# Kernel optimization log

Measured on AMD Instinct MI355X. Metric: run time of the kernel, lower is better.

## Reference

```python
import jax, jax.numpy as jnp
import numpy as np

M, N1, N2, DX, H = 4, 1024, 1024, 3, 64


def setup_inputs() -> dict:
    key = jax.random.key(0)
    ks = jax.random.split(key, 8)
    diff = jax.random.normal(ks[0], (M, N1, N2, DX), dtype=jnp.float32)
    mask = jax.random.randint(ks[1], (M, N1, N2), 0, 2) == 1  # True -> masked out
    W1 = jax.random.normal(ks[2], (DX, H), dtype=jnp.float32) / np.float32(np.sqrt(DX))
    b1 = jnp.zeros((H,), jnp.float32)
    W2 = jax.random.normal(ks[3], (H, H), dtype=jnp.float32) / np.float32(np.sqrt(H))
    b2 = jnp.zeros((H,), jnp.float32)
    W3 = jax.random.normal(ks[4], (H, 1), dtype=jnp.float32) / np.float32(np.sqrt(H))
    b3 = jnp.zeros((1,), jnp.float32)
    return {"diff": diff, "mask": mask, "W1": W1, "b1": b1,
            "W2": W2, "b2": b2, "W3": W3, "b3": b3}


def reference(diff, mask, W1, b1, W2, b2, W3, b3):
    # MLP applied pointwise over [m, n1, n2, dx] -> scalar score per (m, n1, n2)
    h = jax.nn.relu(jnp.einsum("mijd,dh->mijh", diff, W1) + b1)
    h = jax.nn.relu(jnp.einsum("mijh,hk->mijk", h, W2) + b2)
    dots = (jnp.einsum("mijh,ho->mijo", h, W3) + b3)[..., 0]  # [m, n1, n2]
    # masked_fill(mask, -inf) then softmax over n2
    dots = jnp.where(mask, -jnp.inf, dots)
    return jax.nn.softmax(dots, axis=-1)
```

## Files before the change

### kernel.cpp

```cpp
#include <hip/hip_runtime.h>
#include <hip/hip_fp16.h>
#include <math.h>

typedef __attribute__((ext_vector_type(8))) _Float16 half8;
typedef __attribute__((ext_vector_type(2))) __fp16 fp16x2;
typedef __attribute__((ext_vector_type(4))) float float4v;

#define MFMA_F16 __builtin_amdgcn_mfma_f32_16x16x32_f16

__global__ __launch_bounds__(256, 2) void mlp_softmax_kernel(
    const float* __restrict__ diff, const int* __restrict__ mask,
    const float* __restrict__ W1, const float* __restrict__ b1,
    const float* __restrict__ W2, const float* __restrict__ b2,
    const float* __restrict__ W3, float* __restrict__ out)
{
    __shared__ float s_diff[3072];
    __shared__ float s_w2[4096];
    __shared__ float s_w1[192];
    __shared__ float s_b1[64];
    __shared__ float s_b2[64];
    __shared__ float s_w3[64];
    __shared__ float s_dots[1024];
    __shared__ float s_red[8];

    const int tid = threadIdx.x;
    const int bid = blockIdx.x;
    const long row_off = (long)bid * 3072;

    {
        const float4v* gd = (const float4v*)(diff + row_off);
        float4v* sd = (float4v*)s_diff;
        #pragma unroll
        for (int it = 0; it < 3; ++it) sd[tid + 256 * it] = gd[tid + 256 * it];
        const float4v* gw2 = (const float4v*)W2;
        float4v* sw2 = (float4v*)s_w2;
        #pragma unroll
        for (int it = 0; it < 4; ++it) sw2[tid + 256 * it] = gw2[tid + 256 * it];
        if (tid < 48)                    ((float4v*)s_w1)[tid]      = ((const float4v*)W1)[tid];
        else if (tid >= 64 && tid < 80)  ((float4v*)s_b1)[tid - 64] = ((const float4v*)b1)[tid - 64];
        else if (tid >= 80 && tid < 96)  ((float4v*)s_b2)[tid - 80] = ((const float4v*)b2)[tid - 80];
        else if (tid >= 96 && tid < 112) ((float4v*)s_w3)[tid - 96] = ((const float4v*)W3)[tid - 96];
    }
    __syncthreads();

    const int lane = tid & 63;
    const int wv   = tid >> 6;
    const int lg   = lane >> 4;
    const int lr   = lane & 15;

    float w1r[2][3][8], b1r[2][8];
    #pragma unroll
    for (int kh = 0; kh < 2; ++kh) {
        const int hb = kh * 32 + lg * 8;
        #pragma unroll
        for (int e = 0; e < 8; ++e) {
            b1r[kh][e] = s_b1[hb + e];
            #pragma unroll
            for (int d = 0; d < 3; ++d) w1r[kh][d][e] = s_w1[d * 64 + hb + e];
        }
    }
    half8 bfr[4][2];
    #pragma unroll
    for (int nt = 0; nt < 4; ++nt) {
        #pragma unroll
        for (int kh = 0; kh < 2; ++kh) {
            union { fp16x2 h2[4]; half8 h8; } u;
            #pragma unroll
            for (int ep = 0; ep < 4; ++ep) {
                const int k0 = kh * 32 + lg * 8 + ep * 2;
                const float f0 = s_w2[(k0    ) * 64 + nt * 16 + lr];
                const float f1 = s_w2[(k0 + 1) * 64 + nt * 16 + lr];
                u.h2[ep] = __builtin_amdgcn_cvt_pkrtz(f0, f1);
            }
            bfr[nt][kh] = u.h8;
        }
    }
    float b2r[4], w3r[4];
    #pragma unroll
    for (int nt = 0; nt < 4; ++nt) {
        b2r[nt] = s_b2[nt * 16 + lr];
        w3r[nt] = s_w3[nt * 16 + lr];
    }

    const int jw0 = wv * 256;
    for (int t = 0; t < 16; ++t) {
        const int j0 = jw0 + t * 16;
        const int jp = j0 + lr;
        const float x0 = s_diff[jp * 3 + 0];
        const float x1 = s_diff[jp * 3 + 1];
        const float x2 = s_diff[jp * 3 + 2];

        half8 afr[2];
        #pragma unroll
        for (int kh = 0; kh < 2; ++kh) {
            union { fp16x2 h2[4]; half8 h8; } u;
            #pragma unroll
            for (int ep = 0; ep < 4; ++ep) {
                const int e0 = ep * 2, e1 = ep * 2 + 1;
                float h0 = fmaf(x2, w1r[kh][2][e0],
                           fmaf(x1, w1r[kh][1][e0],
                           fmaf(x0, w1r[kh][0][e0], b1r[kh][e0])));
                float h1 = fmaf(x2, w1r[kh][2][e1],
                           fmaf(x1, w1r[kh][1][e1],
                           fmaf(x0, w1r[kh][0][e1], b1r[kh][e1])));
                h0 = fmaxf(h0, 0.0f);
                h1 = fmaxf(h1, 0.0f);
                u.h2[ep] = __builtin_amdgcn_cvt_pkrtz(h0, h1);
            }
            afr[kh] = u.h8;
        }

        float sr[4] = {0.f, 0.f, 0.f, 0.f};
        #pragma unroll
        for (int nt = 0; nt < 4; ++nt) {
            float4v acc = {b2r[nt], b2r[nt], b2r[nt], b2r[nt]};
            acc = MFMA_F16(afr[0], bfr[nt][0], acc, 0, 0, 0);
            acc = MFMA_F16(afr[1], bfr[nt][1], acc, 0, 0, 0);
            #pragma unroll
            for (int r = 0; r < 4; ++r)
                sr[r] = fmaf(fmaxf(acc[r], 0.0f), w3r[nt], sr[r]);
        }
        #pragma unroll
        for (int off = 1; off < 16; off <<= 1) {
            #pragma unroll
            for (int r = 0; r < 4; ++r) sr[r] += __shfl_xor(sr[r], off, 64);
        }
        if (lr == 0) {
            #pragma unroll
            for (int r = 0; r < 4; ++r) s_dots[j0 + lg * 4 + r] = sr[r];
        }
    }
    __syncthreads();

    const int j4 = tid * 4;
    float4v dv = *(const float4v*)&s_dots[j4];
    const int4 mv = *(const int4*)(mask + (long)bid * 1024 + j4);
    const float NINF = -__builtin_inff();
    float d0 = mv.x ? NINF : dv[0];
    float d1 = mv.y ? NINF : dv[1];
    float d2 = mv.z ? NINF : dv[2];
    float d3 = mv.w ? NINF : dv[3];

    float mx = fmaxf(fmaxf(d0, d1), fmaxf(d2, d3));
    #pragma unroll
    for (int off = 1; off < 64; off <<= 1) mx = fmaxf(mx, __shfl_xor(mx, off, 64));
    if (lane == 0) s_red[wv] = mx;
    __syncthreads();
    mx = fmaxf(fmaxf(s_red[0], s_red[1]), fmaxf(s_red[2], s_red[3]));

    const float e0 = mv.x ? 0.0f : __expf(d0 - mx);
    const float e1 = mv.y ? 0.0f : __expf(d1 - mx);
    const float e2 = mv.z ? 0.0f : __expf(d2 - mx);
    const float e3 = mv.w ? 0.0f : __expf(d3 - mx);
    float s = (e0 + e1) + (e2 + e3);
    #pragma unroll
    for (int off = 1; off < 64; off <<= 1) s += __shfl_xor(s, off, 64);
    if (lane == 0) s_red[4 + wv] = s;
    __syncthreads();
    const float tot = (s_red[4] + s_red[5]) + (s_red[6] + s_red[7]);
    const float inv = 1.0f / tot;

    float4v ov = {e0 * inv, e1 * inv, e2 * inv, e3 * inv};
    *(float4v*)(out + (long)bid * 1024 + j4) = ov;
}

extern "C" void kernel_launch(void* const* d_in, const int* in_sizes, int n_in,
                              void* d_out, int out_size, void* d_ws, size_t ws_size,
                              hipStream_t stream) {
    const float* diff = (const float*)d_in[0];
    const int*   mask = (const int*)d_in[1];
    const float* W1   = (const float*)d_in[2];
    const float* b1   = (const float*)d_in[3];
    const float* W2   = (const float*)d_in[4];
    const float* b2   = (const float*)d_in[5];
    const float* W3   = (const float*)d_in[6];
    float* out = (float*)d_out;

    mlp_softmax_kernel<<<dim3(4096), dim3(256), 0, stream>>>(
        diff, mask, W1, b1, W2, b2, W3, out);
}
```

Before: 189.9 us.

## Transpose MFMA operands so hidden units lie along lanes, cutting reduction shuffles

The MFMA operands are swapped so the output tile puts hidden units in the accumulator rows and points in the lanes. The W3 dot product can then be reduced mostly within each lane, which replaces sixteen cross-lane shuffles per tile with two. Layer-1 and W3 arithmetic is vectorised into packed float2 FMAs, and the s_dots buffer now reuses the W2 shared memory after an added barrier, which lowers LDS use. The risks are a wrong operand layout for the swapped MFMA and the extra synchronisation.

```diff
diff --git a/kernel.cpp b/kernel.cpp
--- a/kernel.cpp
+++ b/kernel.cpp
@@ -5,6 +5,7 @@
 typedef __attribute__((ext_vector_type(8))) _Float16 half8;
 typedef __attribute__((ext_vector_type(2))) __fp16 fp16x2;
 typedef __attribute__((ext_vector_type(4))) float float4v;
+typedef __attribute__((ext_vector_type(2))) float float2v;
 
 #define MFMA_F16 __builtin_amdgcn_mfma_f32_16x16x32_f16
 
@@ -20,8 +21,9 @@
     __shared__ float s_b1[64];
     __shared__ float s_b2[64];
     __shared__ float s_w3[64];
-    __shared__ float s_dots[1024];
     __shared__ float s_red[8];
+
+    float* const s_dots = s_w2;
 
     const int tid = threadIdx.x;
     const int bid = blockIdx.x;
@@ -48,15 +50,17 @@
     const int lg   = lane >> 4;
     const int lr   = lane & 15;
 
-    float w1r[2][3][8], b1r[2][8];
+    const int hb0 = lg * 8;
+    float2v w1p[2][3][4], b1p[2][4];
     #pragma unroll
     for (int kh = 0; kh < 2; ++kh) {
-        const int hb = kh * 32 + lg * 8;
+        const int hb = kh * 32 + hb0;
         #pragma unroll
-        for (int e = 0; e < 8; ++e) {
-            b1r[kh][e] = s_b1[hb + e];
+        for (int p = 0; p < 4; ++p) {
+            b1p[kh][p] = *(const float2v*)&s_b1[hb + 2 * p];
             #pragma unroll
-            for (int d = 0; d < 3; ++d) w1r[kh][d][e] = s_w1[d * 64 + hb + e];
+            for (int d = 0; d < 3; ++d)
+                w1p[kh][d][p] = *(const float2v*)&s_w1[d * 64 + hb + 2 * p];
         }
     }
     half8 bfr[4][2];
@@ -75,12 +79,16 @@
             bfr[nt][kh] = u.h8;
         }
     }
-    float b2r[4], w3r[4];
+    float4v b2v[4], w3v[4];
     #pragma unroll
     for (int nt = 0; nt < 4; ++nt) {
-        b2r[nt] = s_b2[nt * 16 + lr];
-        w3r[nt] = s_w3[nt * 16 + lr];
+        b2v[nt] = *(const float4v*)&s_b2[nt * 16 + lg * 4];
+        w3v[nt] = *(const float4v*)&s_w3[nt * 16 + lg * 4];
     }
+    __syncthreads();
+
+    const float2v zero2 = {0.0f, 0.0f};
+    const float4v zero4 = {0.0f, 0.0f, 0.0f, 0.0f};
 
     const int jw0 = wv * 256;
     for (int t = 0; t < 16; ++t) {
@@ -89,46 +97,41 @@
         const float x0 = s_diff[jp * 3 + 0];
         const float x1 = s_diff[jp * 3 + 1];
         const float x2 = s_diff[jp * 3 + 2];
+        const float2v x0p = {x0, x0}, x1p = {x1, x1}, x2p = {x2, x2};
 
         half8 afr[2];
         #pragma unroll
         for (int kh = 0; kh < 2; ++kh) {
             union { fp16x2 h2[4]; half8 h8; } u;
             #pragma unroll
-            for (int ep = 0; ep < 4; ++ep) {
-                const int e0 = ep * 2, e1 = ep * 2 + 1;
-                float h0 = fmaf(x2, w1r[kh][2][e0],
-                           fmaf(x1, w1r[kh][1][e0],
-                           fmaf(x0, w1r[kh][0][e0], b1r[kh][e0])));
-                float h1 = fmaf(x2, w1r[kh][2][e1],
-                           fmaf(x1, w1r[kh][1][e1],
-                           fmaf(x0, w1r[kh][0][e1], b1r[kh][e1])));
-                h0 = fmaxf(h0, 0.0f);
-                h1 = fmaxf(h1, 0.0f);
-                u.h2[ep] = __builtin_amdgcn_cvt_pkrtz(h0, h1);
+            for (int p = 0; p < 4; ++p) {
+                float2v h = b1p[kh][p];
+                h = __builtin_elementwise_fma(x0p, w1p[kh][0][p], h);
+                h = __builtin_elementwise_fma(x1p, w1p[kh][1][p], h);
+                h = __builtin_elementwise_fma(x2p, w1p[kh][2][p], h);
+                h = __builtin_elementwise_max(h, zero2);
+                u.h2[p] = __builtin_amdgcn_cvt_pkrtz(h[0], h[1]);
             }
             afr[kh] = u.h8;
         }
 
-        float sr[4] = {0.f, 0.f, 0.f, 0.f};
+        float2v sr2 = zero2;
         #pragma unroll
         for (int nt = 0; nt < 4; ++nt) {
-            float4v acc = {b2r[nt], b2r[nt], b2r[nt], b2r[nt]};
-            acc = MFMA_F16(afr[0], bfr[nt][0], acc, 0, 0, 0);
-            acc = MFMA_F16(afr[1], bfr[nt][1], acc, 0, 0, 0);
-            #pragma unroll
-            for (int r = 0; r < 4; ++r)
-                sr[r] = fmaf(fmaxf(acc[r], 0.0f), w3r[nt], sr[r]);
+            float4v acc = b2v[nt];
+            acc = MFMA_F16(bfr[nt][0], afr[0], acc, 0, 0, 0);
+            acc = MFMA_F16(bfr[nt][1], afr[1], acc, 0, 0, 0);
+            const float4v rl = __builtin_elementwise_max(acc, zero4);
+            const float2v rlo = {rl[0], rl[1]}, rhi = {rl[2], rl[3]};
+            const float2v wlo = {w3v[nt][0], w3v[nt][1]};
+            const float2v whi = {w3v[nt][2], w3v[nt][3]};
+            sr2 = __builtin_elementwise_fma(rlo, wlo, sr2);
+            sr2 = __builtin_elementwise_fma(rhi, whi, sr2);
         }
-        #pragma unroll
-        for (int off = 1; off < 16; off <<= 1) {
-            #pragma unroll
-            for (int r = 0; r < 4; ++r) sr[r] += __shfl_xor(sr[r], off, 64);
-        }
-        if (lr == 0) {
-            #pragma unroll
-            for (int r = 0; r < 4; ++r) s_dots[j0 + lg * 4 + r] = sr[r];
-        }
+        float sr = sr2[0] + sr2[1];
+        sr += __shfl_xor(sr, 16, 64);
+        sr += __shfl_xor(sr, 32, 64);
+        if (lane < 16) s_dots[j0 + lane] = sr;
     }
     __syncthreads();
 
```

Measured after the change: 169.9 us. 1.12x faster.
